# Performance work log

Hardware: AMD Instinct MI355X
Metric: run time of the kernel (lower is better)

Reference implementation:

```python
import jax, jax.numpy as jnp
import numpy as np

B, C, H, W = 2048, 4, 84, 84
FEAT = 7 * 7 * 64  # 3136, from 84->20->9->7 conv arithmetic
D = 512
E = 6            # num_experts
K = 2            # top_k
A = 12           # output_dim (actions)


def _conv(x, w, b, stride):
    y = jax.lax.conv_general_dilated(
        x, w, window_strides=(stride, stride), padding='VALID',
        dimension_numbers=('NCHW', 'OIHW', 'NCHW'))
    return y + b[None, :, None, None]


def setup_inputs() -> dict:
    key = jax.random.key(0)
    ks = jax.random.split(key, 16)
    s = lambda k, shape, fan: jax.random.normal(k, shape, jnp.float32) * (1.0 / np.sqrt(fan))
    return {
        'x': jax.random.normal(ks[0], (B, C, H, W), jnp.float32),
        'c1_w': s(ks[1], (32, C, 8, 8), C * 64), 'c1_b': jnp.zeros((32,), jnp.float32),
        'c2_w': s(ks[2], (64, 32, 4, 4), 32 * 16), 'c2_b': jnp.zeros((64,), jnp.float32),
        'c3_w': s(ks[3], (64, 64, 3, 3), 64 * 9), 'c3_b': jnp.zeros((64,), jnp.float32),
        'fc_w': s(ks[4], (FEAT, D), FEAT), 'fc_b': jnp.zeros((D,), jnp.float32),
        'gate_w': s(ks[5], (D, E), D), 'gate_b': jnp.zeros((E,), jnp.float32),
        'e_w1': s(ks[6], (E, D, D), D), 'e_b1': jnp.zeros((E, D), jnp.float32),
        'e_w2': s(ks[7], (E, D, D), D), 'e_b2': jnp.zeros((E, D), jnp.float32),
        'e_w3': s(ks[8], (E, D, A), D), 'e_b3': jnp.zeros((E, A), jnp.float32),
    }


def reference(x, c1_w, c1_b, c2_w, c2_b, c3_w, c3_b, fc_w, fc_b,
              gate_w, gate_b, e_w1, e_b1, e_w2, e_b2, e_w3, e_b3):
    # CNN feature extractor (dropout omitted: eval semantics)
    h = jax.nn.relu(_conv(x, c1_w, c1_b, 4))
    h = jax.nn.relu(_conv(h, c2_w, c2_b, 2))
    h = jax.nn.relu(_conv(h, c3_w, c3_b, 1))
    h = h.reshape(h.shape[0], -1)                     # [B, 3136] (C,H,W flatten order)
    f = jax.nn.relu(h @ fc_w + fc_b)                  # [B, 512]

    # Gating: softmax -> top-2 -> renormalize
    gate_probs = jax.nn.softmax(f @ gate_w + gate_b, axis=-1)    # [B, E]
    top_p, top_i = jax.lax.top_k(gate_probs, K)                   # [B, K]
    top_p = top_p / jnp.sum(top_p, axis=-1, keepdims=True)

    # Experts: compute all (tiny MLPs), then gather top-k outputs
    h1 = jax.nn.relu(jnp.einsum('bd,edh->beh', f, e_w1) + e_b1)   # [B, E, D]
    h2 = jax.nn.relu(jnp.einsum('beh,ehg->beg', h1, e_w2) + e_b2) # [B, E, D]
    eo = jnp.einsum('beg,ego->beo', h2, e_w3) + e_b3              # [B, E, A]
    sel = jnp.take_along_axis(eo, top_i[:, :, None], axis=1)      # [B, K, A]
    out = jnp.sum(sel * top_p[:, :, None], axis=1)                # [B, A]
    return out
```

## Files before the change

kernel.cpp:

```cpp
#include <hip/hip_runtime.h>
#include <hip/hip_bf16.h>
#include <math.h>

typedef __attribute__((ext_vector_type(8))) short bf16x8;
typedef __attribute__((ext_vector_type(4))) float f32x4;

__device__ __forceinline__ float b2f(unsigned short u) {
    unsigned int v = ((unsigned int)u) << 16;
    return __uint_as_float(v);
}
__device__ __forceinline__ unsigned short f2b(float f) {
    __hip_bfloat16 h = __float2bfloat16(f);
    return *reinterpret_cast<unsigned short*>(&h);
}
__device__ __forceinline__ void split_trunc(float v, short& h, short& l) {
    unsigned int ui = __float_as_uint(v);
    h = (short)(ui >> 16);
    float hf = __uint_as_float(ui & 0xffff0000u);
    l = (short)f2b(v - hf);
}

__global__ __launch_bounds__(256) void prep_w(
    const float* __restrict__ w1, const float* __restrict__ w2, const float* __restrict__ w3,
    const float* __restrict__ ew3,
    unsigned short* __restrict__ wb1h, unsigned short* __restrict__ wb1l,
    unsigned short* __restrict__ w2h, unsigned short* __restrict__ w2l,
    unsigned short* __restrict__ w3h, unsigned short* __restrict__ w3l,
    float* __restrict__ w3t) {
    int tid = blockIdx.x * 256 + threadIdx.x;
    if (tid < 8192) {
        int k = tid >> 8, r = tid & 255;
        int c = r >> 6, ky = (r >> 3) & 7, kx = r & 7;
        float v = w1[tid];
        unsigned short h = f2b(v);
        int d = ((ky * 2 + (k >> 4)) * 16 + (k & 15)) * 32 + c * 8 + kx;
        wb1h[d] = h;
        wb1l[d] = f2b(v - b2f(h));
    } else if (tid < 8192 + 32768) {
        int i = tid - 8192;
        int n = i >> 9, r = i & 511;
        int c = r >> 4, ky = (r >> 2) & 3, kx = r & 3;
        float v = w2[i];
        unsigned short h = f2b(v);
        int d = ((ky * 4 + kx) * 64 + n) * 32 + c;
        w2h[d] = h;
        w2l[d] = f2b(v - b2f(h));
    } else if (tid < 8192 + 32768 + 36864) {
        int i = tid - 40960;
        int n = i / 576, r = i - n * 576;
        int c = r / 9, s = r - c * 9;
        int ky = s / 3, kx = s - ky * 3;
        float v = w3[i];
        unsigned short h = f2b(v);
        int d = (((ky * 3 + kx) * 2 + (c >> 5)) * 64 + n) * 32 + (c & 31);
        w3h[d] = h;
        w3l[d] = f2b(v - b2f(h));
    } else if (tid < 77824 + 36864) {
        int i = tid - 77824;
        int e = i / 6144, rem = i - e * 6144;
        int a = rem >> 9, k = rem & 511;
        w3t[i] = ew3[e * 6144 + k * 12 + a];
    }
}

__global__ __launch_bounds__(256) void prep_fcw(
    const float* __restrict__ fw, unsigned short* __restrict__ h, unsigned short* __restrict__ l) {
    __shared__ float tile[64][65];
    int k0 = blockIdx.x * 64;
    int n0 = blockIdx.y * 64;
    int tx = threadIdx.x & 63, ty = threadIdx.x >> 6;
#pragma unroll
    for (int j = 0; j < 16; j++) {
        int kk = ty + j * 4;
        int kp = k0 + kk;
        int p = kp >> 6, c = kp & 63;
        tile[kk][tx] = fw[(c * 49 + p) * 512 + n0 + tx];
    }
    __syncthreads();
#pragma unroll
    for (int j = 0; j < 16; j++) {
        int r = ty + j * 4;
        float v = tile[tx][r];
        unsigned short hh = f2b(v);
        long d = (long)(n0 + r) * 3136 + k0 + tx;
        h[d] = hh;
        l[d] = f2b(v - b2f(hh));
    }
}

__global__ __launch_bounds__(256) void prep_ewT(
    const float* __restrict__ ew1, const float* __restrict__ ew2,
    unsigned short* __restrict__ t1, unsigned short* __restrict__ t2) {
    __shared__ float tile[32][33];
    int z = blockIdx.z;
    int e = z % 6;
    const float* src = (z < 6) ? (ew1 + e * 262144) : (ew2 + e * 262144);
    unsigned short* dst = (z < 6) ? (t1 + e * 262144) : (t2 + e * 262144);
    int d0 = blockIdx.y * 32;
    int h0 = blockIdx.x * 32;
    int tx = threadIdx.x, ty = threadIdx.y;
#pragma unroll
    for (int j = 0; j < 4; j++)
        tile[ty + j * 8][tx] = src[(d0 + ty + j * 8) * 512 + h0 + tx];
    __syncthreads();
#pragma unroll
    for (int j = 0; j < 4; j++)
        dst[(h0 + ty + j * 8) * 512 + (d0 + tx)] = f2b(tile[tx][ty + j * 8]);
}

__global__ __launch_bounds__(256) void conv1_k(
    const float* __restrict__ x, const unsigned short* __restrict__ wbh,
    const unsigned short* __restrict__ wbl, const float* __restrict__ b1,
    unsigned short* __restrict__ yhi, unsigned short* __restrict__ ylo) {
    int t = threadIdx.x;
    int wave = t >> 6, lane = t & 63, l16 = lane & 15, quad = lane >> 4;
    int px0 = blockIdx.x * 256 + wave * 64;
    const float* abase[4];
#pragma unroll
    for (int i = 0; i < 4; i++) {
        int px = px0 + i * 16 + l16;
        int n = px / 400;
        int rem = px - n * 400;
        int oy = rem / 20;
        int ox = rem - oy * 20;
        abase[i] = x + (long)n * 28224 + quad * 7056 + oy * 4 * 84 + ox * 4;
    }
    f32x4 acc[4][2];
#pragma unroll
    for (int i = 0; i < 4; i++)
#pragma unroll
        for (int j = 0; j < 2; j++)
#pragma unroll
            for (int r = 0; r < 4; r++) acc[i][j][r] = 0.f;
#pragma unroll
    for (int ky = 0; ky < 8; ky++) {
        bf16x8 ah[4], al[4];
#pragma unroll
        for (int i = 0; i < 4; i++) {
            const float* p = abase[i] + ky * 84;
            float4 v0 = *(const float4*)p;
            float4 v1 = *(const float4*)(p + 4);
            float v[8] = {v0.x, v0.y, v0.z, v0.w, v1.x, v1.y, v1.z, v1.w};
#pragma unroll
            for (int j = 0; j < 8; j++) {
                short hh, ll;
                split_trunc(v[j], hh, ll);
                ah[i][j] = hh;
                al[i][j] = ll;
            }
        }
        int wo = (ky * 2 * 16 + l16) * 32 + quad * 8;
        bf16x8 bh0 = *(const bf16x8*)(wbh + wo);
        bf16x8 bh1 = *(const bf16x8*)(wbh + wo + 512);
        bf16x8 bl0 = *(const bf16x8*)(wbl + wo);
        bf16x8 bl1 = *(const bf16x8*)(wbl + wo + 512);
#pragma unroll
        for (int i = 0; i < 4; i++) {
            acc[i][0] = __builtin_amdgcn_mfma_f32_16x16x32_bf16(ah[i], bh0, acc[i][0], 0, 0, 0);
            acc[i][0] = __builtin_amdgcn_mfma_f32_16x16x32_bf16(al[i], bh0, acc[i][0], 0, 0, 0);
            acc[i][0] = __builtin_amdgcn_mfma_f32_16x16x32_bf16(ah[i], bl0, acc[i][0], 0, 0, 0);
            acc[i][1] = __builtin_amdgcn_mfma_f32_16x16x32_bf16(ah[i], bh1, acc[i][1], 0, 0, 0);
            acc[i][1] = __builtin_amdgcn_mfma_f32_16x16x32_bf16(al[i], bh1, acc[i][1], 0, 0, 0);
            acc[i][1] = __builtin_amdgcn_mfma_f32_16x16x32_bf16(ah[i], bl1, acc[i][1], 0, 0, 0);
        }
    }
    float bias0 = b1[l16], bias1 = b1[16 + l16];
#pragma unroll
    for (int i = 0; i < 4; i++) {
#pragma unroll
        for (int r = 0; r < 4; r++) {
            long px = px0 + i * 16 + quad * 4 + r;
            long o = px * 32;
            float v0 = fmaxf(acc[i][0][r] + bias0, 0.f);
            float v1 = fmaxf(acc[i][1][r] + bias1, 0.f);
            short h0, l0, h1, l1;
            split_trunc(v0, h0, l0);
            split_trunc(v1, h1, l1);
            yhi[o + l16] = (unsigned short)h0;
            ylo[o + l16] = (unsigned short)l0;
            yhi[o + 16 + l16] = (unsigned short)h1;
            ylo[o + 16 + l16] = (unsigned short)l1;
        }
    }
}

template <int C, int IH, int IW, int OH, int OW, int S, int KH, int KW>
__global__ __launch_bounds__(256) void convm_k(
    const unsigned short* __restrict__ xhi, const unsigned short* __restrict__ xlo,
    const unsigned short* __restrict__ whi, const unsigned short* __restrict__ wlo,
    const float* __restrict__ bias,
    unsigned short* __restrict__ yhi, unsigned short* __restrict__ ylo) {
    constexpr int CH = C / 32;
    constexpr int NCHUNK = KH * KW * CH;
    __shared__ unsigned short Ah[256][40], Al[256][40], Bh[64][40], Bl[64][40];
    int t = threadIdx.x;
    int px = blockIdx.x * 256 + t;
    int n = px / (OH * OW);
    int rem = px - n * (OH * OW);
    int oy = rem / OW;
    int ox = rem - oy * OW;
    const long xoff = (((long)n * IH + oy * S) * IW + ox * S) * C;
    int wave = t >> 6, lane = t & 63, l16 = lane & 15, quad = lane >> 4;
    int br = t >> 2, bc = (t & 3) * 8;
    f32x4 acc[4][4];
#pragma unroll
    for (int i = 0; i < 4; i++)
#pragma unroll
        for (int j = 0; j < 4; j++)
#pragma unroll
            for (int r = 0; r < 4; r++) acc[i][j][r] = 0.f;
    for (int ck = 0; ck < NCHUNK; ck++) {
        int kyx = ck / CH;
        int ch = ck - kyx * CH;
        int ky = kyx / KW, kx = kyx - ky * KW;
        long a_src = xoff + ((ky * IW + kx) * C + ch * 32);
#pragma unroll
        for (int j = 0; j < 4; j++) {
            *(bf16x8*)&Ah[t][j * 8] = *(const bf16x8*)(xhi + a_src + j * 8);
            *(bf16x8*)&Al[t][j * 8] = *(const bf16x8*)(xlo + a_src + j * 8);
        }
        long b_src = (long)ck * 2048 + br * 32 + bc;
        *(bf16x8*)&Bh[br][bc] = *(const bf16x8*)(whi + b_src);
        *(bf16x8*)&Bl[br][bc] = *(const bf16x8*)(wlo + b_src);
        __syncthreads();
        bf16x8 ah[4], al[4], bh[4], bl[4];
#pragma unroll
        for (int i = 0; i < 4; i++) {
            ah[i] = *(const bf16x8*)&Ah[wave * 64 + i * 16 + l16][quad * 8];
            al[i] = *(const bf16x8*)&Al[wave * 64 + i * 16 + l16][quad * 8];
            bh[i] = *(const bf16x8*)&Bh[i * 16 + l16][quad * 8];
            bl[i] = *(const bf16x8*)&Bl[i * 16 + l16][quad * 8];
        }
#pragma unroll
        for (int i = 0; i < 4; i++)
#pragma unroll
            for (int j = 0; j < 4; j++) {
                acc[i][j] = __builtin_amdgcn_mfma_f32_16x16x32_bf16(ah[i], bh[j], acc[i][j], 0, 0, 0);
                acc[i][j] = __builtin_amdgcn_mfma_f32_16x16x32_bf16(ah[i], bl[j], acc[i][j], 0, 0, 0);
                acc[i][j] = __builtin_amdgcn_mfma_f32_16x16x32_bf16(al[i], bh[j], acc[i][j], 0, 0, 0);
            }
        __syncthreads();
    }
    int pxbase = blockIdx.x * 256 + wave * 64;
#pragma unroll
    for (int i = 0; i < 4; i++)
#pragma unroll
        for (int j = 0; j < 4; j++) {
            int col = j * 16 + l16;
            float bv = bias[col];
#pragma unroll
            for (int r = 0; r < 4; r++) {
                int prow = pxbase + i * 16 + quad * 4 + r;
                float v = fmaxf(acc[i][j][r] + bv, 0.f);
                unsigned short h = f2b(v);
                yhi[(long)prow * 64 + col] = h;
                ylo[(long)prow * 64 + col] = f2b(v - b2f(h));
            }
        }
}

__global__ __launch_bounds__(256) void fc_k(
    const unsigned short* __restrict__ Ahi, const unsigned short* __restrict__ Alo,
    const unsigned short* __restrict__ Bhi, const unsigned short* __restrict__ Blo,
    float* __restrict__ Cp) {
    __shared__ unsigned short Ash[64][40], Asl[64][40], Bsh[64][40], Bsl[64][40];
    int t = threadIdx.x;
    int m0 = blockIdx.x * 64, n0 = blockIdx.y * 64;
    int z = blockIdx.z;
    int kBase = z * 1568;
    int wave = t >> 6, lane = t & 63, l16 = lane & 15, quad = lane >> 4;
    int wm = (wave & 1) * 32, wn = (wave >> 1) * 32;
    int sr = t >> 2, sk = (t & 3) * 8;
    f32x4 acc[2][2];
#pragma unroll
    for (int i = 0; i < 2; i++)
#pragma unroll
        for (int j = 0; j < 2; j++)
#pragma unroll
            for (int r = 0; r < 4; r++) acc[i][j][r] = 0.f;
    for (int k0 = kBase; k0 < kBase + 1568; k0 += 32) {
        *(bf16x8*)&Ash[sr][sk] = *(const bf16x8*)(Ahi + (long)(m0 + sr) * 3136 + k0 + sk);
        *(bf16x8*)&Asl[sr][sk] = *(const bf16x8*)(Alo + (long)(m0 + sr) * 3136 + k0 + sk);
        *(bf16x8*)&Bsh[sr][sk] = *(const bf16x8*)(Bhi + (long)(n0 + sr) * 3136 + k0 + sk);
        *(bf16x8*)&Bsl[sr][sk] = *(const bf16x8*)(Blo + (long)(n0 + sr) * 3136 + k0 + sk);
        __syncthreads();
        bf16x8 ah[2], al[2], bh[2], bl[2];
#pragma unroll
        for (int i = 0; i < 2; i++) {
            ah[i] = *(const bf16x8*)&Ash[wm + i * 16 + l16][quad * 8];
            al[i] = *(const bf16x8*)&Asl[wm + i * 16 + l16][quad * 8];
            bh[i] = *(const bf16x8*)&Bsh[wn + i * 16 + l16][quad * 8];
            bl[i] = *(const bf16x8*)&Bsl[wn + i * 16 + l16][quad * 8];
        }
#pragma unroll
        for (int i = 0; i < 2; i++)
#pragma unroll
            for (int j = 0; j < 2; j++) {
                acc[i][j] = __builtin_amdgcn_mfma_f32_16x16x32_bf16(ah[i], bh[j], acc[i][j], 0, 0, 0);
                acc[i][j] = __builtin_amdgcn_mfma_f32_16x16x32_bf16(ah[i], bl[j], acc[i][j], 0, 0, 0);
                acc[i][j] = __builtin_amdgcn_mfma_f32_16x16x32_bf16(al[i], bh[j], acc[i][j], 0, 0, 0);
            }
        __syncthreads();
    }
    float* Cz = Cp + (long)z * 1048576;
#pragma unroll
    for (int mt = 0; mt < 2; mt++)
#pragma unroll
        for (int nt = 0; nt < 2; nt++) {
            int col = n0 + wn + nt * 16 + l16;
#pragma unroll
            for (int r = 0; r < 4; r++) {
                int row = m0 + wm + mt * 16 + quad * 4 + r;
                Cz[row * 512 + col] = acc[mt][nt][r];
            }
        }
}

__global__ __launch_bounds__(256) void fc_fin(
    const float* __restrict__ Cp, const float* __restrict__ bias,
    float* __restrict__ f, unsigned short* __restrict__ fb) {
    int tid = blockIdx.x * 256 + threadIdx.x;
    int col = tid & 511;
    float v = Cp[tid] + Cp[tid + 1048576] + bias[col];
    v = fmaxf(v, 0.f);
    f[tid] = v;
    fb[tid] = f2b(v);
}

__global__ __launch_bounds__(256) void gate_k(
    const float* __restrict__ f, const float* __restrict__ gw, const float* __restrict__ gb,
    int* __restrict__ topi, float* __restrict__ topp) {
    int wave = threadIdx.x >> 6, lane = threadIdx.x & 63;
    int row = blockIdx.x * 4 + wave;
    float fv[8];
#pragma unroll
    for (int j = 0; j < 8; j++) fv[j] = f[row * 512 + lane + 64 * j];
    float lg[6];
#pragma unroll
    for (int e = 0; e < 6; e++) {
        float a = 0.f;
#pragma unroll
        for (int j = 0; j < 8; j++) a += fv[j] * gw[(lane + 64 * j) * 6 + e];
#pragma unroll
        for (int off = 32; off > 0; off >>= 1) a += __shfl_xor(a, off, 64);
        lg[e] = a + gb[e];
    }
    if (lane == 0) {
        int i1 = 0;
        float v1 = lg[0];
#pragma unroll
        for (int e = 1; e < 6; e++)
            if (lg[e] > v1) { v1 = lg[e]; i1 = e; }
        int i2 = (i1 == 0) ? 1 : 0;
        float v2 = lg[i2];
#pragma unroll
        for (int e = 0; e < 6; e++)
            if (e != i1 && lg[e] > v2) { v2 = lg[e]; i2 = e; }
        float pa = 1.f / (1.f + expf(v2 - v1));
        topi[row * 2] = i1;
        topi[row * 2 + 1] = i2;
        topp[row * 2] = pa;
        topp[row * 2 + 1] = 1.f - pa;
    }
}

__global__ __launch_bounds__(256) void moe_gemm(
    const unsigned short* __restrict__ A, long aStride,
    const unsigned short* __restrict__ Bt, const float* __restrict__ bias,
    unsigned short* __restrict__ C) {
    int e = blockIdx.z;
    const unsigned short* Ae = A + (long)e * aStride;
    const unsigned short* Be = Bt + (long)e * 262144;
    const float* be = bias + e * 512;
    unsigned short* Ce = C + (long)e * 2048 * 512;
    __shared__ unsigned short As[64 * 40];
    __shared__ unsigned short Bs[64 * 40];
    int t = threadIdx.x;
    int m0 = blockIdx.x * 64, n0 = blockIdx.y * 64;
    int wave = t >> 6, lane = t & 63;
    int l16 = lane & 15, quad = lane >> 4;
    int wm = (wave & 1) * 32, wn = (wave >> 1) * 32;
    int sm = t >> 2, sk = (t & 3) * 8;
    f32x4 acc[2][2];
#pragma unroll
    for (int i = 0; i < 2; i++)
#pragma unroll
        for (int j = 0; j < 2; j++)
#pragma unroll
            for (int r = 0; r < 4; r++) acc[i][j][r] = 0.f;
    for (int k0 = 0; k0 < 512; k0 += 32) {
        bf16x8 av = *(const bf16x8*)&Ae[(long)(m0 + sm) * 512 + k0 + sk];
        bf16x8 bv = *(const bf16x8*)&Be[(long)(n0 + sm) * 512 + k0 + sk];
        *(bf16x8*)&As[sm * 40 + sk] = av;
        *(bf16x8*)&Bs[sm * 40 + sk] = bv;
        __syncthreads();
        bf16x8 af0 = *(const bf16x8*)&As[(wm + l16) * 40 + quad * 8];
        bf16x8 af1 = *(const bf16x8*)&As[(wm + 16 + l16) * 40 + quad * 8];
        bf16x8 bf0 = *(const bf16x8*)&Bs[(wn + l16) * 40 + quad * 8];
        bf16x8 bf1 = *(const bf16x8*)&Bs[(wn + 16 + l16) * 40 + quad * 8];
        acc[0][0] = __builtin_amdgcn_mfma_f32_16x16x32_bf16(af0, bf0, acc[0][0], 0, 0, 0);
        acc[0][1] = __builtin_amdgcn_mfma_f32_16x16x32_bf16(af0, bf1, acc[0][1], 0, 0, 0);
        acc[1][0] = __builtin_amdgcn_mfma_f32_16x16x32_bf16(af1, bf0, acc[1][0], 0, 0, 0);
        acc[1][1] = __builtin_amdgcn_mfma_f32_16x16x32_bf16(af1, bf1, acc[1][1], 0, 0, 0);
        __syncthreads();
    }
#pragma unroll
    for (int mt = 0; mt < 2; mt++)
#pragma unroll
        for (int nt = 0; nt < 2; nt++) {
            int col = n0 + wn + nt * 16 + l16;
            float bcol = be[col];
#pragma unroll
            for (int r = 0; r < 4; r++) {
                int row = m0 + wm + mt * 16 + quad * 4 + r;
                float v = fmaxf(acc[mt][nt][r] + bcol, 0.f);
                Ce[(long)row * 512 + col] = f2b(v);
            }
        }
}

__global__ __launch_bounds__(256) void combine_k(
    const unsigned short* __restrict__ h2, const float* __restrict__ w3t,
    const float* __restrict__ b3, const int* __restrict__ topi,
    const float* __restrict__ topp, float* __restrict__ out) {
    int b = blockIdx.x * 4 + (threadIdx.x >> 6);
    int lane = threadIdx.x & 63;
    int e0 = topi[b * 2], e1 = topi[b * 2 + 1];
    float p0 = topp[b * 2], p1 = topp[b * 2 + 1];
    float r[12];
#pragma unroll
    for (int a = 0; a < 12; a++) r[a] = 0.f;
#pragma unroll
    for (int j = 0; j < 2; j++) {
        int e = j ? e1 : e0;
        float p = j ? p1 : p0;
        const unsigned short* hp = h2 + ((long)e * 2048 + b) * 512 + lane * 8;
        bf16x8 hv = *(const bf16x8*)hp;
        float hf[8];
#pragma unroll
        for (int q = 0; q < 8; q++) hf[q] = b2f((unsigned short)hv[q]);
        const float* wb = w3t + e * 6144 + lane * 8;
#pragma unroll
        for (int a = 0; a < 12; a++) {
            float4 w0 = *(const float4*)(wb + a * 512);
            float4 w1 = *(const float4*)(wb + a * 512 + 4);
            float acc = hf[0] * w0.x + hf[1] * w0.y + hf[2] * w0.z + hf[3] * w0.w +
                        hf[4] * w1.x + hf[5] * w1.y + hf[6] * w1.z + hf[7] * w1.w;
            r[a] += p * acc;
        }
    }
#pragma unroll
    for (int a = 0; a < 12; a++)
#pragma unroll
        for (int off = 32; off > 0; off >>= 1) r[a] += __shfl_xor(r[a], off, 64);
    float v = 0.f;
#pragma unroll
    for (int a = 0; a < 12; a++)
        if (lane == a) v = r[a];
    if (lane < 12)
        out[b * 12 + lane] = v + p0 * b3[e0 * 12 + lane] + p1 * b3[e1 * 12 + lane];
}

extern "C" void kernel_launch(void* const* d_in, const int* in_sizes, int n_in,
                              void* d_out, int out_size, void* d_ws, size_t ws_size,
                              hipStream_t stream) {
    const float* x   = (const float*)d_in[0];
    const float* c1w = (const float*)d_in[1];
    const float* c1b = (const float*)d_in[2];
    const float* c2w = (const float*)d_in[3];
    const float* c2b = (const float*)d_in[4];
    const float* c3w = (const float*)d_in[5];
    const float* c3b = (const float*)d_in[6];
    const float* fcw = (const float*)d_in[7];
    const float* fcb = (const float*)d_in[8];
    const float* gw  = (const float*)d_in[9];
    const float* gb  = (const float*)d_in[10];
    const float* ew1 = (const float*)d_in[11];
    const float* eb1 = (const float*)d_in[12];
    const float* ew2 = (const float*)d_in[13];
    const float* eb2 = (const float*)d_in[14];
    const float* ew3 = (const float*)d_in[15];
    const float* eb3 = (const float*)d_in[16];

    char* ws = (char*)d_ws;
    unsigned short* y1hi = (unsigned short*)(ws + 0L);
    unsigned short* y1lo = (unsigned short*)(ws + 52428800L);
    unsigned short* f3hi = (unsigned short*)(ws + 0L);
    unsigned short* f3lo = (unsigned short*)(ws + 12845056L);
    unsigned short* y2hi = (unsigned short*)(ws + 104857600L);
    unsigned short* y2lo = (unsigned short*)(ws + 126091264L);
    unsigned short* h1   = (unsigned short*)(ws + 104857600L);
    unsigned short* h2   = (unsigned short*)(ws + 117440512L);
    float* f             = (float*)(ws + 147324928L);
    unsigned short* fb   = (unsigned short*)(ws + 151519232L);
    int*   topi          = (int*)(ws + 153616384L);
    float* topp          = (float*)(ws + 153632768L);
    unsigned short* w2h  = (unsigned short*)(ws + 153681920L);
    unsigned short* w2l  = (unsigned short*)(ws + 153747456L);
    unsigned short* w3h  = (unsigned short*)(ws + 153812992L);
    unsigned short* w3l  = (unsigned short*)(ws + 153886720L);
    unsigned short* fcwh = (unsigned short*)(ws + 153960448L);
    unsigned short* fcwl = (unsigned short*)(ws + 157171712L);
    unsigned short* ew1t = (unsigned short*)(ws + 160382976L);
    unsigned short* ew2t = (unsigned short*)(ws + 163528704L);
    float* w3t           = (float*)(ws + 166674432L);
    float* Cp            = (float*)(ws + 166821888L);
    unsigned short* wb1h = (unsigned short*)(ws + 175210496L);
    unsigned short* wb1l = (unsigned short*)(ws + 175226880L);
    float* out = (float*)d_out;

    hipLaunchKernelGGL(prep_w, dim3(448), dim3(256), 0, stream, c1w, c2w, c3w, ew3,
                       wb1h, wb1l, w2h, w2l, w3h, w3l, w3t);
    hipLaunchKernelGGL(prep_fcw, dim3(49, 8), dim3(256), 0, stream, fcw, fcwh, fcwl);
    hipLaunchKernelGGL(prep_ewT, dim3(16, 16, 12), dim3(32, 8), 0, stream, ew1, ew2, ew1t, ew2t);
    hipLaunchKernelGGL(conv1_k, dim3(3200), dim3(256), 0, stream, x, wb1h, wb1l, c1b, y1hi, y1lo);
    hipLaunchKernelGGL((convm_k<32, 20, 20, 9, 9, 2, 4, 4>), dim3(648), dim3(256), 0, stream,
                       y1hi, y1lo, w2h, w2l, c2b, y2hi, y2lo);
    hipLaunchKernelGGL((convm_k<64, 9, 9, 7, 7, 1, 3, 3>), dim3(392), dim3(256), 0, stream,
                       y2hi, y2lo, w3h, w3l, c3b, f3hi, f3lo);
    hipLaunchKernelGGL(fc_k, dim3(32, 8, 2), dim3(256), 0, stream, f3hi, f3lo, fcwh, fcwl, Cp);
    hipLaunchKernelGGL(fc_fin, dim3(4096), dim3(256), 0, stream, Cp, fcb, f, fb);
    hipLaunchKernelGGL(gate_k, dim3(512), dim3(256), 0, stream, f, gw, gb, topi, topp);
    hipLaunchKernelGGL(moe_gemm, dim3(32, 8, 6), dim3(256), 0, stream, fb, 0L, ew1t, eb1, h1);
    hipLaunchKernelGGL(moe_gemm, dim3(32, 8, 6), dim3(256), 0, stream, h1, 1048576L, ew2t, eb2, h2);
    hipLaunchKernelGGL(combine_k, dim3(512), dim3(256), 0, stream, h2, w3t, eb3, topi, topp, out);
}
```

Before: 715.1 us.

## Replace LDS-staged GEMMs with single-wave register-direct MFMA tiles and split-K fc

```diff
diff --git a/kernel.cpp b/kernel.cpp
--- a/kernel.cpp
+++ b/kernel.cpp
@@ -108,7 +108,7 @@
         dst[(h0 + ty + j * 8) * 512 + (d0 + tx)] = f2b(tile[tx][ty + j * 8]);
 }
 
-__global__ __launch_bounds__(256) void conv1_k(
+__global__ __launch_bounds__(256, 3) void conv1_k(
     const float* __restrict__ x, const unsigned short* __restrict__ wbh,
     const unsigned short* __restrict__ wbl, const float* __restrict__ b1,
     unsigned short* __restrict__ yhi, unsigned short* __restrict__ ylo) {
@@ -132,15 +132,33 @@
         for (int j = 0; j < 2; j++)
 #pragma unroll
             for (int r = 0; r < 4; r++) acc[i][j][r] = 0.f;
+    float4 cur[8];
+#pragma unroll
+    for (int i = 0; i < 4; i++) {
+        cur[i * 2] = *(const float4*)abase[i];
+        cur[i * 2 + 1] = *(const float4*)(abase[i] + 4);
+    }
 #pragma unroll
     for (int ky = 0; ky < 8; ky++) {
+        float4 nxt[8];
+        if (ky < 7) {
+#pragma unroll
+            for (int i = 0; i < 4; i++) {
+                const float* p = abase[i] + (ky + 1) * 84;
+                nxt[i * 2] = *(const float4*)p;
+                nxt[i * 2 + 1] = *(const float4*)(p + 4);
+            }
+        }
+        int wo = (ky * 32 + l16) * 32 + quad * 8;
+        bf16x8 bh0 = *(const bf16x8*)(wbh + wo);
+        bf16x8 bh1 = *(const bf16x8*)(wbh + wo + 512);
+        bf16x8 bl0 = *(const bf16x8*)(wbl + wo);
+        bf16x8 bl1 = *(const bf16x8*)(wbl + wo + 512);
         bf16x8 ah[4], al[4];
 #pragma unroll
         for (int i = 0; i < 4; i++) {
-            const float* p = abase[i] + ky * 84;
-            float4 v0 = *(const float4*)p;
-            float4 v1 = *(const float4*)(p + 4);
-            float v[8] = {v0.x, v0.y, v0.z, v0.w, v1.x, v1.y, v1.z, v1.w};
+            float v[8] = {cur[i * 2].x, cur[i * 2].y, cur[i * 2].z, cur[i * 2].w,
+                          cur[i * 2 + 1].x, cur[i * 2 + 1].y, cur[i * 2 + 1].z, cur[i * 2 + 1].w};
 #pragma unroll
             for (int j = 0; j < 8; j++) {
                 short hh, ll;
@@ -149,11 +167,6 @@
                 al[i][j] = ll;
             }
         }
-        int wo = (ky * 2 * 16 + l16) * 32 + quad * 8;
-        bf16x8 bh0 = *(const bf16x8*)(wbh + wo);
-        bf16x8 bh1 = *(const bf16x8*)(wbh + wo + 512);
-        bf16x8 bl0 = *(const bf16x8*)(wbl + wo);
-        bf16x8 bl1 = *(const bf16x8*)(wbl + wo + 512);
 #pragma unroll
         for (int i = 0; i < 4; i++) {
             acc[i][0] = __builtin_amdgcn_mfma_f32_16x16x32_bf16(ah[i], bh0, acc[i][0], 0, 0, 0);
@@ -162,6 +175,10 @@
             acc[i][1] = __builtin_amdgcn_mfma_f32_16x16x32_bf16(ah[i], bh1, acc[i][1], 0, 0, 0);
             acc[i][1] = __builtin_amdgcn_mfma_f32_16x16x32_bf16(al[i], bh1, acc[i][1], 0, 0, 0);
             acc[i][1] = __builtin_amdgcn_mfma_f32_16x16x32_bf16(ah[i], bl1, acc[i][1], 0, 0, 0);
+        }
+        if (ky < 7) {
+#pragma unroll
+            for (int q = 0; q < 8; q++) cur[q] = nxt[q];
         }
     }
     float bias0 = b1[l16], bias1 = b1[16 + l16];
@@ -185,23 +202,25 @@
 }
 
 template <int C, int IH, int IW, int OH, int OW, int S, int KH, int KW>
-__global__ __launch_bounds__(256) void convm_k(
+__global__ __launch_bounds__(64, 3) void convm_k(
     const unsigned short* __restrict__ xhi, const unsigned short* __restrict__ xlo,
     const unsigned short* __restrict__ whi, const unsigned short* __restrict__ wlo,
     const float* __restrict__ bias,
     unsigned short* __restrict__ yhi, unsigned short* __restrict__ ylo) {
     constexpr int CH = C / 32;
     constexpr int NCHUNK = KH * KW * CH;
-    __shared__ unsigned short Ah[256][40], Al[256][40], Bh[64][40], Bl[64][40];
-    int t = threadIdx.x;
-    int px = blockIdx.x * 256 + t;
-    int n = px / (OH * OW);
-    int rem = px - n * (OH * OW);
-    int oy = rem / OW;
-    int ox = rem - oy * OW;
-    const long xoff = (((long)n * IH + oy * S) * IW + ox * S) * C;
-    int wave = t >> 6, lane = t & 63, l16 = lane & 15, quad = lane >> 4;
-    int br = t >> 2, bc = (t & 3) * 8;
+    int lane = threadIdx.x, l16 = lane & 15, quad = lane >> 4;
+    int pxbase = blockIdx.x * 64;
+    long xoff[4];
+#pragma unroll
+    for (int i = 0; i < 4; i++) {
+        int px = pxbase + i * 16 + l16;
+        int n = px / (OH * OW);
+        int rem = px - n * (OH * OW);
+        int oy = rem / OW;
+        int ox = rem - oy * OW;
+        xoff[i] = (((long)n * IH + oy * S) * IW + ox * S) * C + quad * 8;
+    }
     f32x4 acc[4][4];
 #pragma unroll
     for (int i = 0; i < 4; i++)
@@ -209,27 +228,23 @@
         for (int j = 0; j < 4; j++)
 #pragma unroll
             for (int r = 0; r < 4; r++) acc[i][j][r] = 0.f;
+#pragma unroll 2
     for (int ck = 0; ck < NCHUNK; ck++) {
         int kyx = ck / CH;
         int ch = ck - kyx * CH;
         int ky = kyx / KW, kx = kyx - ky * KW;
-        long a_src = xoff + ((ky * IW + kx) * C + ch * 32);
+        long koff = ((long)(ky * IW + kx)) * C + ch * 32;
+        bf16x8 ah[4], al[4], bh[4], bl[4];
+#pragma unroll
+        for (int i = 0; i < 4; i++) {
+            ah[i] = *(const bf16x8*)(xhi + xoff[i] + koff);
+            al[i] = *(const bf16x8*)(xlo + xoff[i] + koff);
+        }
 #pragma unroll
         for (int j = 0; j < 4; j++) {
-            *(bf16x8*)&Ah[t][j * 8] = *(const bf16x8*)(xhi + a_src + j * 8);
-            *(bf16x8*)&Al[t][j * 8] = *(const bf16x8*)(xlo + a_src + j * 8);
-        }
-        long b_src = (long)ck * 2048 + br * 32 + bc;
-        *(bf16x8*)&Bh[br][bc] = *(const bf16x8*)(whi + b_src);
-        *(bf16x8*)&Bl[br][bc] = *(const bf16x8*)(wlo + b_src);
-        __syncthreads();
-        bf16x8 ah[4], al[4], bh[4], bl[4];
-#pragma unroll
-        for (int i = 0; i < 4; i++) {
-            ah[i] = *(const bf16x8*)&Ah[wave * 64 + i * 16 + l16][quad * 8];
-            al[i] = *(const bf16x8*)&Al[wave * 64 + i * 16 + l16][quad * 8];
-            bh[i] = *(const bf16x8*)&Bh[i * 16 + l16][quad * 8];
-            bl[i] = *(const bf16x8*)&Bl[i * 16 + l16][quad * 8];
+            long b = ((long)ck * 64 + j * 16 + l16) * 32 + quad * 8;
+            bh[j] = *(const bf16x8*)(whi + b);
+            bl[j] = *(const bf16x8*)(wlo + b);
         }
 #pragma unroll
         for (int i = 0; i < 4; i++)
@@ -239,9 +254,7 @@
                 acc[i][j] = __builtin_amdgcn_mfma_f32_16x16x32_bf16(ah[i], bl[j], acc[i][j], 0, 0, 0);
                 acc[i][j] = __builtin_amdgcn_mfma_f32_16x16x32_bf16(al[i], bh[j], acc[i][j], 0, 0, 0);
             }
-        __syncthreads();
-    }
-    int pxbase = blockIdx.x * 256 + wave * 64;
+    }
 #pragma unroll
     for (int i = 0; i < 4; i++)
 #pragma unroll
@@ -259,59 +272,55 @@
         }
 }
 
-__global__ __launch_bounds__(256) void fc_k(
+__global__ __launch_bounds__(64, 3) void fc_k(
     const unsigned short* __restrict__ Ahi, const unsigned short* __restrict__ Alo,
     const unsigned short* __restrict__ Bhi, const unsigned short* __restrict__ Blo,
     float* __restrict__ Cp) {
-    __shared__ unsigned short Ash[64][40], Asl[64][40], Bsh[64][40], Bsl[64][40];
-    int t = threadIdx.x;
+    int lane = threadIdx.x, l16 = lane & 15, quad = lane >> 4;
     int m0 = blockIdx.x * 64, n0 = blockIdx.y * 64;
     int z = blockIdx.z;
-    int kBase = z * 1568;
-    int wave = t >> 6, lane = t & 63, l16 = lane & 15, quad = lane >> 4;
-    int wm = (wave & 1) * 32, wn = (wave >> 1) * 32;
-    int sr = t >> 2, sk = (t & 3) * 8;
-    f32x4 acc[2][2];
-#pragma unroll
-    for (int i = 0; i < 2; i++)
-#pragma unroll
-        for (int j = 0; j < 2; j++)
+    int kBase = z * 448;
+    f32x4 acc[4][4];
+#pragma unroll
+    for (int i = 0; i < 4; i++)
+#pragma unroll
+        for (int j = 0; j < 4; j++)
 #pragma unroll
             for (int r = 0; r < 4; r++) acc[i][j][r] = 0.f;
-    for (int k0 = kBase; k0 < kBase + 1568; k0 += 32) {
-        *(bf16x8*)&Ash[sr][sk] = *(const bf16x8*)(Ahi + (long)(m0 + sr) * 3136 + k0 + sk);
-        *(bf16x8*)&Asl[sr][sk] = *(const bf16x8*)(Alo + (long)(m0 + sr) * 3136 + k0 + sk);
-        *(bf16x8*)&Bsh[sr][sk] = *(const bf16x8*)(Bhi + (long)(n0 + sr) * 3136 + k0 + sk);
-        *(bf16x8*)&Bsl[sr][sk] = *(const bf16x8*)(Blo + (long)(n0 + sr) * 3136 + k0 + sk);
-        __syncthreads();
-        bf16x8 ah[2], al[2], bh[2], bl[2];
-#pragma unroll
-        for (int i = 0; i < 2; i++) {
-            ah[i] = *(const bf16x8*)&Ash[wm + i * 16 + l16][quad * 8];
-            al[i] = *(const bf16x8*)&Asl[wm + i * 16 + l16][quad * 8];
-            bh[i] = *(const bf16x8*)&Bsh[wn + i * 16 + l16][quad * 8];
-            bl[i] = *(const bf16x8*)&Bsl[wn + i * 16 + l16][quad * 8];
-        }
-#pragma unroll
-        for (int i = 0; i < 2; i++)
-#pragma unroll
-            for (int j = 0; j < 2; j++) {
+#pragma unroll 2
+    for (int k0 = kBase; k0 < kBase + 448; k0 += 32) {
+        bf16x8 ah[4], al[4], bh[4], bl[4];
+#pragma unroll
+        for (int i = 0; i < 4; i++) {
+            long a = (long)(m0 + i * 16 + l16) * 3136 + k0 + quad * 8;
+            ah[i] = *(const bf16x8*)(Ahi + a);
+            al[i] = *(const bf16x8*)(Alo + a);
+        }
+#pragma unroll
+        for (int j = 0; j < 4; j++) {
+            long b = (long)(n0 + j * 16 + l16) * 3136 + k0 + quad * 8;
+            bh[j] = *(const bf16x8*)(Bhi + b);
+            bl[j] = *(const bf16x8*)(Blo + b);
+        }
+#pragma unroll
+        for (int i = 0; i < 4; i++)
+#pragma unroll
+            for (int j = 0; j < 4; j++) {
                 acc[i][j] = __builtin_amdgcn_mfma_f32_16x16x32_bf16(ah[i], bh[j], acc[i][j], 0, 0, 0);
                 acc[i][j] = __builtin_amdgcn_mfma_f32_16x16x32_bf16(ah[i], bl[j], acc[i][j], 0, 0, 0);
                 acc[i][j] = __builtin_amdgcn_mfma_f32_16x16x32_bf16(al[i], bh[j], acc[i][j], 0, 0, 0);
             }
-        __syncthreads();
     }
     float* Cz = Cp + (long)z * 1048576;
 #pragma unroll
-    for (int mt = 0; mt < 2; mt++)
-#pragma unroll
-        for (int nt = 0; nt < 2; nt++) {
-            int col = n0 + wn + nt * 16 + l16;
+    for (int i = 0; i < 4; i++)
+#pragma unroll
+        for (int j = 0; j < 4; j++) {
+            int col = n0 + j * 16 + l16;
 #pragma unroll
             for (int r = 0; r < 4; r++) {
-                int row = m0 + wm + mt * 16 + quad * 4 + r;
-                Cz[row * 512 + col] = acc[mt][nt][r];
+                int row = m0 + i * 16 + quad * 4 + r;
+                Cz[row * 512 + col] = acc[i][j][r];
             }
         }
 }
@@ -321,7 +330,9 @@
     float* __restrict__ f, unsigned short* __restrict__ fb) {
     int tid = blockIdx.x * 256 + threadIdx.x;
     int col = tid & 511;
-    float v = Cp[tid] + Cp[tid + 1048576] + bias[col];
+    float v = bias[col];
+#pragma unroll
+    for (int z = 0; z < 7; z++) v += Cp[tid + (long)z * 1048576];
     v = fmaxf(v, 0.f);
     f[tid] = v;
     fb[tid] = f2b(v);
@@ -364,7 +375,7 @@
     }
 }
 
-__global__ __launch_bounds__(256) void moe_gemm(
+__global__ __launch_bounds__(64, 4) void moe_gemm(
     const unsigned short* __restrict__ A, long aStride,
     const unsigned short* __restrict__ Bt, const float* __restrict__ bias,
     unsigned short* __restrict__ C) {
@@ -373,47 +384,40 @@
     const unsigned short* Be = Bt + (long)e * 262144;
     const float* be = bias + e * 512;
     unsigned short* Ce = C + (long)e * 2048 * 512;
-    __shared__ unsigned short As[64 * 40];
-    __shared__ unsigned short Bs[64 * 40];
-    int t = threadIdx.x;
+    int lane = threadIdx.x, l16 = lane & 15, quad = lane >> 4;
     int m0 = blockIdx.x * 64, n0 = blockIdx.y * 64;
-    int wave = t >> 6, lane = t & 63;
-    int l16 = lane & 15, quad = lane >> 4;
-    int wm = (wave & 1) * 32, wn = (wave >> 1) * 32;
-    int sm = t >> 2, sk = (t & 3) * 8;
-    f32x4 acc[2][2];
-#pragma unroll
-    for (int i = 0; i < 2; i++)
-#pragma unroll
-        for (int j = 0; j < 2; j++)
+    f32x4 acc[4][4];
+#pragma unroll
+    for (int i = 0; i < 4; i++)
+#pragma unroll
+        for (int j = 0; j < 4; j++)
 #pragma unroll
             for (int r = 0; r < 4; r++) acc[i][j][r] = 0.f;
+#pragma unroll 4
     for (int k0 = 0; k0 < 512; k0 += 32) {
-        bf16x8 av = *(const bf16x8*)&Ae[(long)(m0 + sm) * 512 + k0 + sk];
-        bf16x8 bv = *(const bf16x8*)&Be[(long)(n0 + sm) * 512 + k0 + sk];
-        *(bf16x8*)&As[sm * 40 + sk] = av;
-        *(bf16x8*)&Bs[sm * 40 + sk] = bv;
-        __syncthreads();
-        bf16x8 af0 = *(const bf16x8*)&As[(wm + l16) * 40 + quad * 8];
-        bf16x8 af1 = *(const bf16x8*)&As[(wm + 16 + l16) * 40 + quad * 8];
-        bf16x8 bf0 = *(const bf16x8*)&Bs[(wn + l16) * 40 + quad * 8];
-        bf16x8 bf1 = *(const bf16x8*)&Bs[(wn + 16 + l16) * 40 + quad * 8];
-        acc[0][0] = __builtin_amdgcn_mfma_f32_16x16x32_bf16(af0, bf0, acc[0][0], 0, 0, 0);
-        acc[0][1] = __builtin_amdgcn_mfma_f32_16x16x32_bf16(af0, bf1, acc[0][1], 0, 0, 0);
-        acc[1][0] = __builtin_amdgcn_mfma_f32_16x16x32_bf16(af1, bf0, acc[1][0], 0, 0, 0);
-        acc[1][1] = __builtin_amdgcn_mfma_f32_16x16x32_bf16(af1, bf1, acc[1][1], 0, 0, 0);
-        __syncthreads();
-    }
-#pragma unroll
-    for (int mt = 0; mt < 2; mt++)
-#pragma unroll
-        for (int nt = 0; nt < 2; nt++) {
-            int col = n0 + wn + nt * 16 + l16;
+        bf16x8 a[4], b[4];
+#pragma unroll
+        for (int i = 0; i < 4; i++)
+            a[i] = *(const bf16x8*)(Ae + (long)(m0 + i * 16 + l16) * 512 + k0 + quad * 8);
+#pragma unroll
+        for (int j = 0; j < 4; j++)
+            b[j] = *(const bf16x8*)(Be + (long)(n0 + j * 16 + l16) * 512 + k0 + quad * 8);
+#pragma unroll
+        for (int i = 0; i < 4; i++)
+#pragma unroll
+            for (int j = 0; j < 4; j++)
+                acc[i][j] = __builtin_amdgcn_mfma_f32_16x16x32_bf16(a[i], b[j], acc[i][j], 0, 0, 0);
+    }
+#pragma unroll
+    for (int i = 0; i < 4; i++)
+#pragma unroll
+        for (int j = 0; j < 4; j++) {
+            int col = n0 + j * 16 + l16;
             float bcol = be[col];
 #pragma unroll
             for (int r = 0; r < 4; r++) {
-                int row = m0 + wm + mt * 16 + quad * 4 + r;
-                float v = fmaxf(acc[mt][nt][r] + bcol, 0.f);
+                int row = m0 + i * 16 + quad * 4 + r;
+                float v = fmaxf(acc[i][j][r] + bcol, 0.f);
                 Ce[(long)row * 512 + col] = f2b(v);
             }
         }
@@ -505,8 +509,8 @@
     unsigned short* ew2t = (unsigned short*)(ws + 163528704L);
     float* w3t           = (float*)(ws + 166674432L);
     float* Cp            = (float*)(ws + 166821888L);
-    unsigned short* wb1h = (unsigned short*)(ws + 175210496L);
-    unsigned short* wb1l = (unsigned short*)(ws + 175226880L);
+    unsigned short* wb1h = (unsigned short*)(ws + 196182016L);
+    unsigned short* wb1l = (unsigned short*)(ws + 196198400L);
     float* out = (float*)d_out;
 
     hipLaunchKernelGGL(prep_w, dim3(448), dim3(256), 0, stream, c1w, c2w, c3w, ew3,
@@ -514,14 +518,14 @@
     hipLaunchKernelGGL(prep_fcw, dim3(49, 8), dim3(256), 0, stream, fcw, fcwh, fcwl);
     hipLaunchKernelGGL(prep_ewT, dim3(16, 16, 12), dim3(32, 8), 0, stream, ew1, ew2, ew1t, ew2t);
     hipLaunchKernelGGL(conv1_k, dim3(3200), dim3(256), 0, stream, x, wb1h, wb1l, c1b, y1hi, y1lo);
-    hipLaunchKernelGGL((convm_k<32, 20, 20, 9, 9, 2, 4, 4>), dim3(648), dim3(256), 0, stream,
+    hipLaunchKernelGGL((convm_k<32, 20, 20, 9, 9, 2, 4, 4>), dim3(2592), dim3(64), 0, stream,
                        y1hi, y1lo, w2h, w2l, c2b, y2hi, y2lo);
-    hipLaunchKernelGGL((convm_k<64, 9, 9, 7, 7, 1, 3, 3>), dim3(392), dim3(256), 0, stream,
+    hipLaunchKernelGGL((convm_k<64, 9, 9, 7, 7, 1, 3, 3>), dim3(1568), dim3(64), 0, stream,
                        y2hi, y2lo, w3h, w3l, c3b, f3hi, f3lo);
-    hipLaunchKernelGGL(fc_k, dim3(32, 8, 2), dim3(256), 0, stream, f3hi, f3lo, fcwh, fcwl, Cp);
+    hipLaunchKernelGGL(fc_k, dim3(32, 8, 7), dim3(64), 0, stream, f3hi, f3lo, fcwh, fcwl, Cp);
     hipLaunchKernelGGL(fc_fin, dim3(4096), dim3(256), 0, stream, Cp, fcb, f, fb);
     hipLaunchKernelGGL(gate_k, dim3(512), dim3(256), 0, stream, f, gw, gb, topi, topp);
-    hipLaunchKernelGGL(moe_gemm, dim3(32, 8, 6), dim3(256), 0, stream, fb, 0L, ew1t, eb1, h1);
-    hipLaunchKernelGGL(moe_gemm, dim3(32, 8, 6), dim3(256), 0, stream, h1, 1048576L, ew2t, eb2, h2);
+    hipLaunchKernelGGL(moe_gemm, dim3(32, 8, 6), dim3(64), 0, stream, fb, 0L, ew1t, eb1, h1);
+    hipLaunchKernelGGL(moe_gemm, dim3(32, 8, 6), dim3(64), 0, stream, h1, 1048576L, ew2t, eb2, h2);
     hipLaunchKernelGGL(combine_k, dim3(512), dim3(256), 0, stream, h2, w3t, eb3, topi, topp, out);
 }
```

Result: no change. 712.0 us (-0.4%).
